# Optimization experiments

Measured on AMD Instinct MI355X. Metric: run time of the kernel, lower is better.

The kernel has to match this reference:

```python
import math
import jax, jax.numpy as jnp
import numpy as np

B, N, C_IN, C_OUT = 16, 1024, 256, 256


def setup_inputs() -> dict:
    key = jax.random.key(0)
    k_x, k_q, k_k, k_v, k_s, k_e = jax.random.split(key, 6)
    x = jax.random.normal(k_x, (B, N, C_IN), dtype=jnp.float32)
    # torch Linear(in, out, bias=False) == x @ W with W: [in, out]
    sc = 1.0 / math.sqrt(C_IN)
    W_q = jax.random.normal(k_q, (C_IN, C_OUT), dtype=jnp.float32) * sc
    W_k = jax.random.normal(k_k, (C_IN, C_OUT), dtype=jnp.float32) * sc
    W_v = jax.random.normal(k_v, (C_IN, C_OUT), dtype=jnp.float32) * sc
    W_sigma = jax.random.normal(k_s, (C_IN, 1), dtype=jnp.float32) * sc
    # fixed standard-normal noise replacing torch.normal's on-the-fly sampling
    eps = jax.random.normal(k_e, (B, N, N), dtype=jnp.float32)
    return {"x": x, "W_q": W_q, "W_k": W_k, "W_v": W_v,
            "W_sigma": W_sigma, "eps": eps}


def reference(x, W_q, W_k, W_v, W_sigma, eps):
    n = x.shape[1]
    d_model = W_q.shape[1]
    Q = x @ W_q            # [B, n, d]
    K = x @ W_k            # [B, n, d]
    V = x @ W_v            # [B, n, d]
    sigma = x @ W_sigma    # [B, n, 1]

    # prior association: gaussian = Normal(mean=|i-j|, std=|sigma|), row-normalized
    idx = jnp.arange(n)
    p = jnp.abs(idx[:, None] - idx[None, :]).astype(x.dtype)   # [n, n]
    gaussian = p[None, :, :] + jnp.abs(sigma) * eps            # [B, n, n]
    P = gaussian / jnp.sum(gaussian, axis=-1, keepdims=True)

    # series association: softmax over dim=0 (batch), exactly as the torch code
    scores = jnp.einsum('bnd,bmd->bnm', Q, K) / math.sqrt(d_model)
    S = jax.nn.softmax(scores, axis=0)

    Z = jnp.einsum('bnm,bmd->bnd', S, V)                       # reconstruction
    return Z, P, S
```

## Files before the change

kernel.cpp:

```cpp
#include <hip/hip_runtime.h>
#include <hip/hip_bf16.h>
#include <math.h>

#define B_ 16
#define N_ 1024
#define C_ 256

typedef unsigned short ushort_t;
typedef __attribute__((ext_vector_type(8))) short short8;
typedef __attribute__((ext_vector_type(4))) float f32x4;

static __device__ __forceinline__ ushort_t f2bf(float f) {
    __hip_bfloat16 h = __float2bfloat16(f);
    return *(ushort_t*)&h;
}

static __device__ __forceinline__ void async16(const ushort_t* g, ushort_t* l) {
    __builtin_amdgcn_global_load_lds(
        (const __attribute__((address_space(1))) unsigned int*)g,
        (__attribute__((address_space(3))) unsigned int*)l,
        16, 0, 0);
}

template <int OUT_BF16>
__global__ __launch_bounds__(256) void gemm_nt_bf16(
    const ushort_t* __restrict__ A, const ushort_t* __restrict__ B,
    void* __restrict__ Cp, int M, int N, int K,
    long sA, long sB, long sC, float alpha)
{
    A += (long)blockIdx.z * sA;
    B += (long)blockIdx.z * sB;

    __shared__ ushort_t sh[2 * 128 * 32];
    ushort_t* As = sh;
    ushort_t* Bs = sh + 128 * 32;
    float* shF = (float*)sh;

    const int tid  = threadIdx.x;
    const int wave = tid >> 6;
    const int lane = tid & 63;
    const int wm   = wave >> 1;
    const int wn   = wave & 1;
    const int row0 = blockIdx.y * 128;
    const int col0 = blockIdx.x * 128;

    const int r_grp = lane >> 2;
    const int c_chk = lane & 3;
    const int swz   = c_chk ^ ((r_grp >> 1) & 3);
    const int ga0 = wave * 2, ga1 = wave * 2 + 1;

    const ushort_t* agp0 = A + (long)(row0 + ga0 * 16 + r_grp) * K + swz * 8;
    const ushort_t* agp1 = A + (long)(row0 + ga1 * 16 + r_grp) * K + swz * 8;
    const ushort_t* bgp0 = B + (long)(col0 + ga0 * 16 + r_grp) * K + swz * 8;
    const ushort_t* bgp1 = B + (long)(col0 + ga1 * 16 + r_grp) * K + swz * 8;
    ushort_t* lA0 = &As[ga0 * 512];
    ushort_t* lA1 = &As[ga1 * 512];
    ushort_t* lB0 = &Bs[ga0 * 512];
    ushort_t* lB1 = &Bs[ga1 * 512];

    const int lr16 = lane & 15;
    const int q16  = lane >> 4;
    const int slot = (q16 ^ ((lr16 >> 1) & 3)) * 8;

    f32x4 acc[4][4] = {};

    for (int k0 = 0; k0 < K; k0 += 32) {
        async16(agp0 + k0, lA0);
        async16(agp1 + k0, lA1);
        async16(bgp0 + k0, lB0);
        async16(bgp1 + k0, lB1);
        __syncthreads();

        short8 av[4], bv[4];
#pragma unroll
        for (int i = 0; i < 4; i++)
            av[i] = *(const short8*)&As[(wm * 64 + i * 16 + lr16) * 32 + slot];
#pragma unroll
        for (int j = 0; j < 4; j++)
            bv[j] = *(const short8*)&Bs[(wn * 64 + j * 16 + lr16) * 32 + slot];

#pragma unroll
        for (int i = 0; i < 4; i++)
#pragma unroll
            for (int j = 0; j < 4; j++)
                acc[i][j] = __builtin_amdgcn_mfma_f32_16x16x32_bf16(
                    av[i], bv[j], acc[i][j], 0, 0, 0);

        __syncthreads();
    }

#pragma unroll
    for (int i = 0; i < 4; i++) {
#pragma unroll
        for (int j = 0; j < 4; j++) {
            const int rl = wm * 16 + q16 * 4;
            const int cl = wn * 64 + j * 16 + lr16;
#pragma unroll
            for (int r = 0; r < 4; r++) {
                const int rr = rl + r;
                const int xr = ((rr >> 2) & 1) << 4;
                shF[rr * 128 + (cl ^ xr)] = alpha * acc[i][j][r];
            }
        }
        __syncthreads();

        if constexpr (OUT_BF16) {
            ushort_t* C = (ushort_t*)Cp + (long)blockIdx.z * sC;
#pragma unroll
            for (int v = 0; v < 2; v++) {
                const int idx = v * 256 + tid;
                const int rl = idx >> 4;
                const int c8 = idx & 15;
                const int xr4 = ((rl >> 2) & 1) << 2;
                const int gr = row0 + (rl >> 4) * 64 + i * 16 + (rl & 15);
                const float4 a = ((const float4*)(shF + rl * 128))[(c8 * 2) ^ xr4];
                const float4 b = ((const float4*)(shF + rl * 128))[(c8 * 2 + 1) ^ xr4];
                short8 pk;
                pk[0] = (short)f2bf(a.x); pk[1] = (short)f2bf(a.y);
                pk[2] = (short)f2bf(a.z); pk[3] = (short)f2bf(a.w);
                pk[4] = (short)f2bf(b.x); pk[5] = (short)f2bf(b.y);
                pk[6] = (short)f2bf(b.z); pk[7] = (short)f2bf(b.w);
                *(short8*)(C + (long)gr * N + col0 + c8 * 8) = pk;
            }
        } else {
            float* C = (float*)Cp + (long)blockIdx.z * sC;
#pragma unroll
            for (int v = 0; v < 4; v++) {
                const int idx = v * 256 + tid;
                const int rl = idx >> 5;
                const int c4 = idx & 31;
                const int xr4 = ((rl >> 2) & 1) << 2;
                const int gr = row0 + (rl >> 4) * 64 + i * 16 + (rl & 15);
                const float4 val = ((const float4*)(shF + rl * 128))[c4 ^ xr4];
                *(float4*)(C + (long)gr * N + col0 + c4 * 4) = val;
            }
        }
        __syncthreads();
    }
}

__global__ __launch_bounds__(256) void cast_x_kernel(
    const float* __restrict__ x, ushort_t* __restrict__ xbf)
{
    const long i = ((long)blockIdx.x * 256 + threadIdx.x) * 4;
    const float4 v = *(const float4*)(x + i);
    ushort4 o;
    o.x = f2bf(v.x); o.y = f2bf(v.y); o.z = f2bf(v.z); o.w = f2bf(v.w);
    *(ushort4*)(xbf + i) = o;
}

__global__ __launch_bounds__(256) void cast_w_kernel(
    const float* __restrict__ Wq, const float* __restrict__ Wk,
    const float* __restrict__ Wv, ushort_t* __restrict__ WbfT)
{
    __shared__ float t[32][33];
    const float* W = (blockIdx.z == 0) ? Wq : (blockIdx.z == 1) ? Wk : Wv;
    const int n0 = blockIdx.x * 32, k0 = blockIdx.y * 32;
    const int tx = threadIdx.x & 31, ty = threadIdx.x >> 5;
#pragma unroll
    for (int j = 0; j < 4; j++)
        t[ty + j * 8][tx] = W[(long)(k0 + ty + j * 8) * 256 + n0 + tx];
    __syncthreads();
    ushort_t* o = WbfT + (long)blockIdx.z * 65536;
#pragma unroll
    for (int j = 0; j < 4; j++)
        o[(long)(n0 + ty + j * 8) * 256 + k0 + tx] = f2bf(t[tx][ty + j * 8]);
}

__global__ __launch_bounds__(256) void transpose_v_kernel(
    const ushort_t* __restrict__ V, ushort_t* __restrict__ VT)
{
    __shared__ ushort_t t[32][33];
    const long NC = (long)N_ * C_;
    const ushort_t* Vb = V + (long)blockIdx.z * NC;
    ushort_t* Tb = VT + (long)blockIdx.z * NC;
    const int n0 = blockIdx.x * 32, m0 = blockIdx.y * 32;
    const int tx = threadIdx.x & 31, ty = threadIdx.x >> 5;
#pragma unroll
    for (int j = 0; j < 4; j++)
        t[ty + j * 8][tx] = Vb[(long)(m0 + ty + j * 8) * C_ + n0 + tx];
    __syncthreads();
#pragma unroll
    for (int j = 0; j < 4; j++)
        Tb[(long)(n0 + ty + j * 8) * N_ + m0 + tx] = t[tx][ty + j * 8];
}

__global__ __launch_bounds__(256) void softmax_batch(
    float* __restrict__ S, ushort_t* __restrict__ Sbf)
{
    const long NN = (long)N_ * N_;
    const long i4 = ((long)blockIdx.x * 256 + threadIdx.x) * 4;

    float4 v[B_];
    float mx = -INFINITY, my = -INFINITY, mz = -INFINITY, mw = -INFINITY;
#pragma unroll
    for (int b = 0; b < B_; b++) {
        v[b] = *(const float4*)(S + (long)b * NN + i4);
        mx = fmaxf(mx, v[b].x); my = fmaxf(my, v[b].y);
        mz = fmaxf(mz, v[b].z); mw = fmaxf(mw, v[b].w);
    }
    float sx = 0.f, sy = 0.f, sz = 0.f, sw = 0.f;
#pragma unroll
    for (int b = 0; b < B_; b++) {
        v[b].x = __expf(v[b].x - mx); sx += v[b].x;
        v[b].y = __expf(v[b].y - my); sy += v[b].y;
        v[b].z = __expf(v[b].z - mz); sz += v[b].z;
        v[b].w = __expf(v[b].w - mw); sw += v[b].w;
    }
    const float ix = 1.0f / sx, iy = 1.0f / sy, iz = 1.0f / sz, iw = 1.0f / sw;
#pragma unroll
    for (int b = 0; b < B_; b++) {
        float4 o;
        o.x = v[b].x * ix; o.y = v[b].y * iy;
        o.z = v[b].z * iz; o.w = v[b].w * iw;
        *(float4*)(S + (long)b * NN + i4) = o;
        ushort4 ob;
        ob.x = f2bf(o.x); ob.y = f2bf(o.y); ob.z = f2bf(o.z); ob.w = f2bf(o.w);
        *(ushort4*)(Sbf + (long)b * NN + i4) = ob;
    }
}

__device__ __forceinline__ float block_reduce_sum(float v, float* red)
{
#pragma unroll
    for (int off = 32; off; off >>= 1) v += __shfl_down(v, off, 64);
    __syncthreads();
    if ((threadIdx.x & 63) == 0) red[threadIdx.x >> 6] = v;
    __syncthreads();
    return red[0] + red[1] + red[2] + red[3];
}

__global__ __launch_bounds__(256) void p_kernel(
    const float* __restrict__ x, const float* __restrict__ Wsig,
    const float* __restrict__ eps, float* __restrict__ P)
{
    __shared__ float red[4];
    const int bn = blockIdx.x;
    const int n = bn & (N_ - 1);
    const int tid = threadIdx.x;

    const float sig = block_reduce_sum(x[(long)bn * C_ + tid] * Wsig[tid], red);
    const float asig = fabsf(sig);

    const float* erow = eps + (long)bn * N_;
    const float4 e = *(const float4*)(erow + tid * 4);
    const int j0 = tid * 4;
    const float g0 = (float)abs(n - (j0 + 0)) + asig * e.x;
    const float g1 = (float)abs(n - (j0 + 1)) + asig * e.y;
    const float g2 = (float)abs(n - (j0 + 2)) + asig * e.z;
    const float g3 = (float)abs(n - (j0 + 3)) + asig * e.w;

    const float total = block_reduce_sum(g0 + g1 + g2 + g3, red);
    const float inv = 1.0f / total;

    float4 o;
    o.x = g0 * inv; o.y = g1 * inv; o.z = g2 * inv; o.w = g3 * inv;
    *(float4*)(P + (long)bn * N_ + j0) = o;
}

extern "C" void kernel_launch(void* const* d_in, const int* in_sizes, int n_in,
                              void* d_out, int out_size, void* d_ws, size_t ws_size,
                              hipStream_t stream)
{
    const float* x    = (const float*)d_in[0];
    const float* Wq   = (const float*)d_in[1];
    const float* Wk   = (const float*)d_in[2];
    const float* Wv   = (const float*)d_in[3];
    const float* Wsig = (const float*)d_in[4];
    const float* eps  = (const float*)d_in[5];
    float* out = (float*)d_out;

    const long ZN = (long)B_ * N_ * C_;
    const long PN = (long)B_ * N_ * N_;
    const long NC = (long)N_ * C_;
    const long NN = (long)N_ * N_;

    float* Zp = out;
    float* Pp = out + ZN;
    float* Sp = out + ZN + PN;

    ushort_t* base = (ushort_t*)Pp;
    ushort_t* Qbf  = base;
    ushort_t* Kbf  = base + ZN;
    ushort_t* Vbf  = base + 2 * ZN;
    ushort_t* xbf  = base + 3 * ZN;
    ushort_t* VbfT = base + 3 * ZN;
    ushort_t* WbfT = base + 4 * ZN;
    ushort_t* Sbf  = base + 4 * ZN;

    const dim3 blk(256);

    cast_x_kernel<<<dim3((B_ * N_ * C_) / 1024), blk, 0, stream>>>(x, xbf);
    cast_w_kernel<<<dim3(8, 8, 3), blk, 0, stream>>>(Wq, Wk, Wv, WbfT);

    gemm_nt_bf16<1><<<dim3(2, 128, 3), blk, 0, stream>>>(
        xbf, WbfT, Qbf, B_ * N_, C_, C_, 0, 65536, ZN, 1.0f);

    transpose_v_kernel<<<dim3(8, 32, 16), blk, 0, stream>>>(Vbf, VbfT);

    gemm_nt_bf16<0><<<dim3(8, 8, 16), blk, 0, stream>>>(
        Qbf, Kbf, Sp, N_, N_, C_, NC, NC, NN, 0.0625f);

    softmax_batch<<<dim3(NN / 1024), blk, 0, stream>>>(Sp, Sbf);

    gemm_nt_bf16<0><<<dim3(2, 8, 16), blk, 0, stream>>>(
        Sbf, VbfT, Zp, N_, C_, N_, NN, NC, NC, 1.0f);

    p_kernel<<<dim3(B_ * N_), blk, 0, stream>>>(x, Wsig, eps, Pp);
}
```

Measured before the change: 305.5 us.

## Double-buffer GEMM LDS, store scores as bf16, fuse casts and sigma

The GEMM main loop now uses two LDS buffers, so the next K-tile is prefetched while the current one is multiplied, and only one barrier is needed per iteration. The QK^T GEMM writes bf16 scores into a scratch area instead of fp32 S, so the softmax reads half the bytes and then writes the final fp32 S plus the bf16 copy in place. The x and W cast kernels merge into one launch that also computes |sigma| into the workspace, so the P kernel skips its per-row reduction. The trade-offs are slightly lower score precision before the softmax, twice the LDS per GEMM block, and a dependence on workspace size for the sigma path.

```diff
diff --git a/kernel.cpp b/kernel.cpp
--- a/kernel.cpp
+++ b/kernel.cpp
@@ -13,6 +13,10 @@
 static __device__ __forceinline__ ushort_t f2bf(float f) {
     __hip_bfloat16 h = __float2bfloat16(f);
     return *(ushort_t*)&h;
+}
+
+static __device__ __forceinline__ float bf2f(ushort_t u) {
+    return __uint_as_float(((unsigned int)u) << 16);
 }
 
 static __device__ __forceinline__ void async16(const ushort_t* g, ushort_t* l) {
@@ -31,9 +35,7 @@
     A += (long)blockIdx.z * sA;
     B += (long)blockIdx.z * sB;
 
-    __shared__ ushort_t sh[2 * 128 * 32];
-    ushort_t* As = sh;
-    ushort_t* Bs = sh + 128 * 32;
+    __shared__ ushort_t sh[2][2 * 128 * 32];
     float* shF = (float*)sh;
 
     const int tid  = threadIdx.x;
@@ -53,10 +55,6 @@
     const ushort_t* agp1 = A + (long)(row0 + ga1 * 16 + r_grp) * K + swz * 8;
     const ushort_t* bgp0 = B + (long)(col0 + ga0 * 16 + r_grp) * K + swz * 8;
     const ushort_t* bgp1 = B + (long)(col0 + ga1 * 16 + r_grp) * K + swz * 8;
-    ushort_t* lA0 = &As[ga0 * 512];
-    ushort_t* lA1 = &As[ga1 * 512];
-    ushort_t* lB0 = &Bs[ga0 * 512];
-    ushort_t* lB1 = &Bs[ga1 * 512];
 
     const int lr16 = lane & 15;
     const int q16  = lane >> 4;
@@ -64,13 +62,29 @@
 
     f32x4 acc[4][4] = {};
 
+    {
+        ushort_t* As = sh[0];
+        ushort_t* Bs = sh[0] + 128 * 32;
+        async16(agp0, &As[ga0 * 512]);
+        async16(agp1, &As[ga1 * 512]);
+        async16(bgp0, &Bs[ga0 * 512]);
+        async16(bgp1, &Bs[ga1 * 512]);
+    }
+    __syncthreads();
+
+    int p = 0;
     for (int k0 = 0; k0 < K; k0 += 32) {
-        async16(agp0 + k0, lA0);
-        async16(agp1 + k0, lA1);
-        async16(bgp0 + k0, lB0);
-        async16(bgp1 + k0, lB1);
-        __syncthreads();
-
+        if (k0 + 32 < K) {
+            ushort_t* As = sh[p ^ 1];
+            ushort_t* Bs = sh[p ^ 1] + 128 * 32;
+            async16(agp0 + k0 + 32, &As[ga0 * 512]);
+            async16(agp1 + k0 + 32, &As[ga1 * 512]);
+            async16(bgp0 + k0 + 32, &Bs[ga0 * 512]);
+            async16(bgp1 + k0 + 32, &Bs[ga1 * 512]);
+        }
+
+        const ushort_t* As = sh[p];
+        const ushort_t* Bs = sh[p] + 128 * 32;
         short8 av[4], bv[4];
 #pragma unroll
         for (int i = 0; i < 4; i++)
@@ -87,6 +101,7 @@
                     av[i], bv[j], acc[i][j], 0, 0, 0);
 
         __syncthreads();
+        p ^= 1;
     }
 
 #pragma unroll
@@ -139,32 +154,43 @@
     }
 }
 
-__global__ __launch_bounds__(256) void cast_x_kernel(
-    const float* __restrict__ x, ushort_t* __restrict__ xbf)
-{
-    const long i = ((long)blockIdx.x * 256 + threadIdx.x) * 4;
-    const float4 v = *(const float4*)(x + i);
-    ushort4 o;
-    o.x = f2bf(v.x); o.y = f2bf(v.y); o.z = f2bf(v.z); o.w = f2bf(v.w);
-    *(ushort4*)(xbf + i) = o;
-}
-
-__global__ __launch_bounds__(256) void cast_w_kernel(
+__global__ __launch_bounds__(256) void cast_fused(
+    const float* __restrict__ x, ushort_t* __restrict__ xbf,
     const float* __restrict__ Wq, const float* __restrict__ Wk,
-    const float* __restrict__ Wv, ushort_t* __restrict__ WbfT)
+    const float* __restrict__ Wv, ushort_t* __restrict__ WbfT,
+    const float* __restrict__ Wsig, float* __restrict__ asig)
 {
     __shared__ float t[32][33];
-    const float* W = (blockIdx.z == 0) ? Wq : (blockIdx.z == 1) ? Wk : Wv;
-    const int n0 = blockIdx.x * 32, k0 = blockIdx.y * 32;
-    const int tx = threadIdx.x & 31, ty = threadIdx.x >> 5;
-#pragma unroll
-    for (int j = 0; j < 4; j++)
-        t[ty + j * 8][tx] = W[(long)(k0 + ty + j * 8) * 256 + n0 + tx];
-    __syncthreads();
-    ushort_t* o = WbfT + (long)blockIdx.z * 65536;
-#pragma unroll
-    for (int j = 0; j < 4; j++)
-        o[(long)(n0 + ty + j * 8) * 256 + k0 + tx] = f2bf(t[tx][ty + j * 8]);
+    const int blk = blockIdx.x;
+    if (blk < 4096) {
+        const long i = ((long)blk * 256 + threadIdx.x) * 4;
+        const float4 v = *(const float4*)(x + i);
+        ushort4 o;
+        o.x = f2bf(v.x); o.y = f2bf(v.y); o.z = f2bf(v.z); o.w = f2bf(v.w);
+        *(ushort4*)(xbf + i) = o;
+        if (asig) {
+            const int lane = threadIdx.x & 63;
+            const float4 w = *(const float4*)(Wsig + lane * 4);
+            float d = v.x * w.x + v.y * w.y + v.z * w.z + v.w * w.w;
+#pragma unroll
+            for (int off = 32; off; off >>= 1) d += __shfl_down(d, off, 64);
+            if (lane == 0) asig[blk * 4 + (threadIdx.x >> 6)] = fabsf(d);
+        }
+    } else {
+        const int m = blk - 4096;
+        const float* W = ((m >> 6) == 0) ? Wq : ((m >> 6) == 1) ? Wk : Wv;
+        const int rem = m & 63;
+        const int n0 = (rem & 7) * 32, k0 = (rem >> 3) * 32;
+        const int tx = threadIdx.x & 31, ty = threadIdx.x >> 5;
+#pragma unroll
+        for (int j = 0; j < 4; j++)
+            t[ty + j * 8][tx] = W[(long)(k0 + ty + j * 8) * 256 + n0 + tx];
+        __syncthreads();
+        ushort_t* o = WbfT + (long)(m >> 6) * 65536;
+#pragma unroll
+        for (int j = 0; j < 4; j++)
+            o[(long)(n0 + ty + j * 8) * 256 + k0 + tx] = f2bf(t[tx][ty + j * 8]);
+    }
 }
 
 __global__ __launch_bounds__(256) void transpose_v_kernel(
@@ -186,7 +212,7 @@
 }
 
 __global__ __launch_bounds__(256) void softmax_batch(
-    float* __restrict__ S, ushort_t* __restrict__ Sbf)
+    ushort_t* __restrict__ Sc, float* __restrict__ S)
 {
     const long NN = (long)N_ * N_;
     const long i4 = ((long)blockIdx.x * 256 + threadIdx.x) * 4;
@@ -195,7 +221,9 @@
     float mx = -INFINITY, my = -INFINITY, mz = -INFINITY, mw = -INFINITY;
 #pragma unroll
     for (int b = 0; b < B_; b++) {
-        v[b] = *(const float4*)(S + (long)b * NN + i4);
+        const ushort4 u = *(const ushort4*)(Sc + (long)b * NN + i4);
+        v[b].x = bf2f(u.x); v[b].y = bf2f(u.y);
+        v[b].z = bf2f(u.z); v[b].w = bf2f(u.w);
         mx = fmaxf(mx, v[b].x); my = fmaxf(my, v[b].y);
         mz = fmaxf(mz, v[b].z); mw = fmaxf(mw, v[b].w);
     }
@@ -216,7 +244,7 @@
         *(float4*)(S + (long)b * NN + i4) = o;
         ushort4 ob;
         ob.x = f2bf(o.x); ob.y = f2bf(o.y); ob.z = f2bf(o.z); ob.w = f2bf(o.w);
-        *(ushort4*)(Sbf + (long)b * NN + i4) = ob;
+        *(ushort4*)(Sc + (long)b * NN + i4) = ob;
     }
 }
 
@@ -232,23 +260,28 @@
 
 __global__ __launch_bounds__(256) void p_kernel(
     const float* __restrict__ x, const float* __restrict__ Wsig,
-    const float* __restrict__ eps, float* __restrict__ P)
+    const float* __restrict__ eps, float* __restrict__ P,
+    const float* __restrict__ asig)
 {
     __shared__ float red[4];
     const int bn = blockIdx.x;
     const int n = bn & (N_ - 1);
     const int tid = threadIdx.x;
 
-    const float sig = block_reduce_sum(x[(long)bn * C_ + tid] * Wsig[tid], red);
-    const float asig = fabsf(sig);
+    float a;
+    if (asig) {
+        a = asig[bn];
+    } else {
+        a = fabsf(block_reduce_sum(x[(long)bn * C_ + tid] * Wsig[tid], red));
+    }
 
     const float* erow = eps + (long)bn * N_;
     const float4 e = *(const float4*)(erow + tid * 4);
     const int j0 = tid * 4;
-    const float g0 = (float)abs(n - (j0 + 0)) + asig * e.x;
-    const float g1 = (float)abs(n - (j0 + 1)) + asig * e.y;
-    const float g2 = (float)abs(n - (j0 + 2)) + asig * e.z;
-    const float g3 = (float)abs(n - (j0 + 3)) + asig * e.w;
+    const float g0 = (float)abs(n - (j0 + 0)) + a * e.x;
+    const float g1 = (float)abs(n - (j0 + 1)) + a * e.y;
+    const float g2 = (float)abs(n - (j0 + 2)) + a * e.z;
+    const float g3 = (float)abs(n - (j0 + 3)) + a * e.w;
 
     const float total = block_reduce_sum(g0 + g1 + g2 + g3, red);
     const float inv = 1.0f / total;
@@ -286,25 +319,28 @@
     ushort_t* xbf  = base + 3 * ZN;
     ushort_t* VbfT = base + 3 * ZN;
     ushort_t* WbfT = base + 4 * ZN;
-    ushort_t* Sbf  = base + 4 * ZN;
+    ushort_t* Scbf = base + 4 * ZN;
+
+    float* asig = (ws_size >= (size_t)(B_ * N_) * sizeof(float))
+                      ? (float*)d_ws : nullptr;
 
     const dim3 blk(256);
 
-    cast_x_kernel<<<dim3((B_ * N_ * C_) / 1024), blk, 0, stream>>>(x, xbf);
-    cast_w_kernel<<<dim3(8, 8, 3), blk, 0, stream>>>(Wq, Wk, Wv, WbfT);
+    cast_fused<<<dim3(4096 + 192), blk, 0, stream>>>(
+        x, xbf, Wq, Wk, Wv, WbfT, Wsig, asig);
 
     gemm_nt_bf16<1><<<dim3(2, 128, 3), blk, 0, stream>>>(
         xbf, WbfT, Qbf, B_ * N_, C_, C_, 0, 65536, ZN, 1.0f);
 
     transpose_v_kernel<<<dim3(8, 32, 16), blk, 0, stream>>>(Vbf, VbfT);
 
-    gemm_nt_bf16<0><<<dim3(8, 8, 16), blk, 0, stream>>>(
-        Qbf, Kbf, Sp, N_, N_, C_, NC, NC, NN, 0.0625f);
-
-    softmax_batch<<<dim3(NN / 1024), blk, 0, stream>>>(Sp, Sbf);
+    gemm_nt_bf16<1><<<dim3(8, 8, 16), blk, 0, stream>>>(
+        Qbf, Kbf, Scbf, N_, N_, C_, NC, NC, NN, 0.0625f);
+
+    softmax_batch<<<dim3(NN / 1024), blk, 0, stream>>>(Scbf, Sp);
 
     gemm_nt_bf16<0><<<dim3(2, 8, 16), blk, 0, stream>>>(
-        Sbf, VbfT, Zp, N_, C_, N_, NN, NC, NC, 1.0f);
-
-    p_kernel<<<dim3(B_ * N_), blk, 0, stream>>>(x, Wsig, eps, Pp);
-}
+        Scbf, VbfT, Zp, N_, C_, N_, NN, NC, NC, 1.0f);
+
+    p_kernel<<<dim3(B_ * N_), blk, 0, stream>>>(x, Wsig, eps, Pp, asig);
+}
```

New measurement: 287.9 us. 1.06x faster.
